# Optimization experiments

Hardware: AMD Instinct MI355X
Metric: run time of the kernel (lower is better)

Reference implementation:

```python
import jax, jax.numpy as jnp
import numpy as np

N_E = 8192
E_DIM = 512
BETA = 0.25


def setup_inputs() -> dict:
    key = jax.random.key(0)
    k1, k2, k3, k4, k5 = jax.random.split(key, 5)
    B, C, T = 8, E_DIM, 1024
    z = jax.random.normal(k1, (B, C, T), dtype=jnp.float32)
    # domain ids: 0 (speech), 1 (music), 2 (audio), 3 (no restriction / else-branch)
    audio_domain = jax.random.randint(k2, (B,), 0, 4, dtype=jnp.int64)
    # frozen codebook, init N(0, e_dim^-0.5) as in nn.init.normal_
    emb_weight = jax.random.normal(k3, (N_E, E_DIM), dtype=jnp.float32) * (E_DIM ** -0.5)
    # embedding_proj = nn.Linear(e_dim, e_dim): weight [out,in], bias [out]
    lim = 1.0 / np.sqrt(E_DIM)
    proj_w = jax.random.uniform(k4, (E_DIM, E_DIM), minval=-lim, maxval=lim, dtype=jnp.float32)
    proj_b = jax.random.uniform(k5, (E_DIM,), minval=-lim, maxval=lim, dtype=jnp.float32)
    return {"z": z, "audio_domain": audio_domain, "n_q": 1,
            "emb_weight": emb_weight, "proj_w": proj_w, "proj_b": proj_b}


def _domain_valid_mask(audio_domain):
    # valid[b, n] = True if code n is allowed for sample b
    cs = N_E // 4
    idx = jnp.arange(N_E)                      # [n_e]
    dom = audio_domain[:, None]                # [B, 1]
    m0 = idx < cs                              # domain 0: first quarter
    m1 = (idx >= cs) & (idx < 2 * cs)          # domain 1: second quarter
    m2 = idx >= 2 * cs                         # domain 2: last half
    valid = jnp.where(dom == 0, m0[None, :],
            jnp.where(dom == 1, m1[None, :],
            jnp.where(dom == 2, m2[None, :], True)))
    return valid                               # [B, n_e] bool


def reference(z, audio_domain, n_q, emb_weight, proj_w, proj_b):
    B, C, T = z.shape
    zt = jnp.transpose(z, (0, 2, 1))                       # [B, T, e_dim]
    zf = zt.reshape(-1, E_DIM)                              # [B*T, e_dim]
    # quant_codebook = Linear(embedding.weight)
    codebook = emb_weight @ proj_w.T + proj_b               # [n_e, e_dim]
    # squared euclidean distances via sum-sq + matmul
    d = (jnp.sum(zf * zf, axis=1, keepdims=True)
         + jnp.sum(codebook * codebook, axis=1)[None, :]
         - 2.0 * jnp.einsum('bd,nd->bn', zf, codebook))     # [B*T, n_e]
    d = d.reshape(B, T, N_E)
    valid = _domain_valid_mask(audio_domain)                # [B, n_e]
    d = jnp.where(valid[:, None, :], d, jnp.inf)
    min_idx = jnp.argmin(d, axis=2)                         # [B, T]
    z_q = codebook[min_idx]                                 # [B, T, e_dim]
    sg = jax.lax.stop_gradient
    # legacy=True commit loss
    commit_loss = (jnp.mean((sg(z_q) - zt) ** 2)
                   + BETA * jnp.mean((z_q - sg(zt)) ** 2))
    z_q = zt + sg(z_q - zt)                                 # straight-through
    z_q = jnp.transpose(z_q, (0, 2, 1))                     # [B, e_dim, T]
    min_idx = min_idx.reshape(1, B, T)                      # sane_index_shape
    return z_q, min_idx, commit_loss
```

## Files before the change

### kernel.cpp

```cpp
#include <hip/hip_runtime.h>
#include <math.h>

#define NE   8192
#define ED   512
#define BB   8
#define TT   1024
#define MM   (BB*TT)

#define FLT_BIG 3.402823466e38f
#define MARGIN  0.08f

typedef _Float16 half8 __attribute__((ext_vector_type(8)));
typedef _Float16 half4 __attribute__((ext_vector_type(4)));
typedef float    floatx4 __attribute__((ext_vector_type(4)));

typedef __attribute__((address_space(3))) unsigned int       lds_u32;
typedef const __attribute__((address_space(1))) unsigned int gbl_u32;

__device__ __forceinline__ void async_copy16(void* lds, const void* g) {
    __builtin_amdgcn_global_load_lds((gbl_u32*)(unsigned long long)g,
                                     (lds_u32*)(unsigned long long)lds,
                                     16, 0, 0);
}

__global__ __launch_bounds__(256) void k_prep(
    const float* __restrict__ z, const float* __restrict__ emb,
    const float* __restrict__ pw, _Float16* __restrict__ Zh,
    float* __restrict__ Zt, _Float16* __restrict__ Eb,
    _Float16* __restrict__ Wb, float* __restrict__ cnorm)
{
    const int bid = blockIdx.x;
    const int tid = threadIdx.x;
    if (bid < 1024) {
        __shared__ float T[64][68];
        const int ct = bid & 7, tt = (bid >> 3) & 15, b = bid >> 7;
        const int f4 = tid & 15;
        const int c0 = tid >> 4;
#pragma unroll
        for (int r = 0; r < 4; ++r) {
            const int c = c0 + r * 16;
            const float4 v = *(const float4*)(z + ((size_t)(b * ED + ct * 64 + c)) * TT + tt * 64 + f4 * 4);
            T[f4*4+0][c] = v.x; T[f4*4+1][c] = v.y;
            T[f4*4+2][c] = v.z; T[f4*4+3][c] = v.w;
        }
        __syncthreads();
        {
            const int tl = tid >> 2, q = tid & 3;
            const size_t m = (size_t)b * TT + tt * 64 + tl;
            _Float16* outh = Zh + m * 512 + ct * 64 + q * 16;
#pragma unroll
            for (int g = 0; g < 2; ++g) {
                half8 hv;
#pragma unroll
                for (int jj = 0; jj < 8; ++jj)
                    hv[jj] = (_Float16)(4.0f * T[tl][q*16 + g*8 + jj]);
                *(half8*)(outh + g * 8) = hv;
            }
        }
        {
            const int tl2 = tid >> 4;
            const int c4 = (tid & 15) * 4;
#pragma unroll
            for (int it = 0; it < 4; ++it) {
                const int t_local = tl2 + it * 16;
                const float4 v = *(const float4*)&T[t_local][c4];
                *(float4*)(Zt + ((size_t)b * TT + tt * 64 + t_local) * 512 + ct * 64 + c4) = v;
            }
        }
    } else if (bid < 5376) {
        const int g = (bid - 1024) * 256 + tid;
        const int row = g >> 7, c4 = (g & 127) * 4;
        const float* src;
        _Float16* dst;
        if (row < NE) { src = emb + (size_t)row * 512;        dst = Eb + (size_t)row * 1024; }
        else          { src = pw + (size_t)(row - NE) * 512;  dst = Wb + (size_t)(row - NE) * 1024; }
        const float4 v = *(const float4*)(src + c4);
        half4 h, l;
        const float s[4] = {v.x * 64.0f, v.y * 64.0f, v.z * 64.0f, v.w * 64.0f};
#pragma unroll
        for (int j = 0; j < 4; ++j) {
            const _Float16 hh = (_Float16)s[j];
            h[j] = hh;
            l[j] = (_Float16)(s[j] - (float)hh);
        }
        *(half4*)(dst + c4) = h;
        *(half4*)(dst + 512 + c4) = l;
    } else {
        const int zidx = bid - 5376;
        if (zidx < 8) {
            ((float4*)cnorm)[zidx * 256 + tid] = make_float4(0.f, 0.f, 0.f, 0.f);
        } else if (tid == 0) {
            cnorm[NE] = 0.0f;
            ((unsigned int*)cnorm)[NE + 1] = 0u;
        }
    }
}

#define S_AH 0
#define S_AL 8192
#define S_BH 16384
#define S_BL 20480
__global__ __launch_bounds__(256) void k_cb(
    const _Float16* __restrict__ Eb, const _Float16* __restrict__ Wb,
    const float* __restrict__ pb, float* __restrict__ cb,
    _Float16* __restrict__ Ch, float* __restrict__ cnorm)
{
    __shared__ __align__(16) _Float16 S[24576];

    const int tid = threadIdx.x;
    const int wave = tid >> 6, lane = tid & 63;
    const int n0 = blockIdx.x * 128, d0 = blockIdx.y * 64;
    const int wm = wave >> 1, wn = wave & 1;
    const int lm = lane & 15, lq = lane >> 4;

    floatx4 acc[4][2];
#pragma unroll
    for (int i = 0; i < 4; ++i)
#pragma unroll
        for (int j = 0; j < 2; ++j) acc[i][j] = (floatx4)0.0f;

    for (int lc = 0; lc < 8; ++lc) {
        const int kc = lc * 64;
        __syncthreads();
#pragma unroll
        for (int r = 0; r < 12; ++r) {
            const int s = wave * 12 + r;
            const int row8 = lane >> 3;
            const int srcx = lane & 7;
            if (s < 16) {
                const int row = s * 8 + row8;
                const int src = srcx ^ (row & 7);
                async_copy16(&S[S_AH + s * 512], Eb + (size_t)(n0 + row) * 1024 + kc + src * 8);
            } else if (s < 32) {
                const int s2 = s - 16;
                const int row = s2 * 8 + row8;
                const int src = srcx ^ (row & 7);
                async_copy16(&S[S_AL + s2 * 512], Eb + (size_t)(n0 + row) * 1024 + 512 + kc + src * 8);
            } else if (s < 40) {
                const int s2 = s - 32;
                const int row = s2 * 8 + row8;
                const int src = srcx ^ (row & 7);
                async_copy16(&S[S_BH + s2 * 512], Wb + (size_t)(d0 + row) * 1024 + kc + src * 8);
            } else {
                const int s2 = s - 40;
                const int row = s2 * 8 + row8;
                const int src = srcx ^ (row & 7);
                async_copy16(&S[S_BL + s2 * 512], Wb + (size_t)(d0 + row) * 1024 + 512 + kc + src * 8);
            }
        }
        __syncthreads();

#pragma unroll
        for (int ks = 0; ks < 2; ++ks) {
            half8 ah[4], al[4], bh[2], bl[2];
#pragma unroll
            for (int i = 0; i < 4; ++i) {
                const int row = wm * 64 + i * 16 + lm;
                const int slot = (ks * 4 + lq) ^ (row & 7);
                ah[i] = *(const half8*)&S[S_AH + row * 64 + slot * 8];
                al[i] = *(const half8*)&S[S_AL + row * 64 + slot * 8];
            }
#pragma unroll
            for (int j = 0; j < 2; ++j) {
                const int row = wn * 32 + j * 16 + lm;
                const int slot = (ks * 4 + lq) ^ (row & 7);
                bh[j] = *(const half8*)&S[S_BH + row * 64 + slot * 8];
                bl[j] = *(const half8*)&S[S_BL + row * 64 + slot * 8];
            }
#pragma unroll
            for (int i = 0; i < 4; ++i)
#pragma unroll
                for (int j = 0; j < 2; ++j) {
                    acc[i][j] = __builtin_amdgcn_mfma_f32_16x16x32_f16(ah[i], bh[j], acc[i][j], 0, 0, 0);
                    acc[i][j] = __builtin_amdgcn_mfma_f32_16x16x32_f16(ah[i], bl[j], acc[i][j], 0, 0, 0);
                    acc[i][j] = __builtin_amdgcn_mfma_f32_16x16x32_f16(al[i], bh[j], acc[i][j], 0, 0, 0);
                }
        }
    }

    float bias[2];
#pragma unroll
    for (int j = 0; j < 2; ++j) bias[j] = pb[d0 + wn * 32 + j * 16 + lm];

    float nsum[16];
#pragma unroll
    for (int p = 0; p < 16; ++p) nsum[p] = 0.0f;

#pragma unroll
    for (int i = 0; i < 4; ++i) {
#pragma unroll
        for (int j = 0; j < 2; ++j) {
            const int d = d0 + wn * 32 + j * 16 + lm;
#pragma unroll
            for (int r = 0; r < 4; ++r) {
                const float v = acc[i][j][r] * 0.000244140625f + bias[j];
                const int n = n0 + wm * 64 + i * 16 + lq * 4 + r;
                cb[(size_t)n * 512 + d] = v;
                Ch[(size_t)n * 512 + d] = (_Float16)(v * 64.0f);
                nsum[i * 4 + r] += v * v;
            }
        }
    }
#pragma unroll
    for (int stp = 1; stp < 16; stp <<= 1) {
#pragma unroll
        for (int p = 0; p < 16; ++p) nsum[p] += __shfl_xor(nsum[p], stp);
    }
    float myv = nsum[0];
#pragma unroll
    for (int p = 1; p < 16; ++p) if (lm == p) myv = nsum[p];
    const int n = n0 + wm * 64 + (lm >> 2) * 16 + lq * 4 + (lm & 3);
    atomicAdd(&cnorm[n], myv);
}

__global__ __launch_bounds__(256) void k_coarse(
    const _Float16* __restrict__ Zh, const _Float16* __restrict__ Ch,
    const float* __restrict__ cnorm, const int* __restrict__ dom_arr,
    _Float16* __restrict__ bmin)
{
    const int mt = blockIdx.x;
    const int nt = blockIdx.y;
    const int b = mt >> 3;
    const int dom = dom_arr[b];
    const int chunk = nt >> 4;
    const bool valid = (dom == 3) || (dom == 0 && chunk == 0) ||
                       (dom == 1 && chunk == 1) || (dom == 2 && chunk >= 2);

    const int tid = threadIdx.x;
    const int m0 = mt * 128, n0 = nt * 128;

    if (!valid) {
        const int r = tid >> 1, h = tid & 1;
        half8 v;
#pragma unroll
        for (int k = 0; k < 8; ++k) v[k] = (_Float16)65504.0f;
        *(half8*)(bmin + (size_t)(m0 + r) * 1024 + nt * 16 + h * 8) = v;
        return;
    }

    __shared__ __align__(16) _Float16 As[128 * 64];
    __shared__ __align__(16) _Float16 Bs[128 * 64];
    __shared__ __align__(16) _Float16 bs[128][20];
    __shared__ __align__(16) float cnLds[128];

    const int wave = tid >> 6, lane = tid & 63;
    const int wm = wave >> 1, wn = wave & 1;
    const int lm = lane & 15, lq = lane >> 4;

    floatx4 acc[4][4];
#pragma unroll
    for (int i = 0; i < 4; ++i)
#pragma unroll
        for (int j = 0; j < 4; ++j) acc[i][j] = (floatx4)0.0f;

    for (int lc = 0; lc < 8; ++lc) {
        const int kk0 = lc * 64;
        __syncthreads();
#pragma unroll
        for (int r = 0; r < 4; ++r) {
            const int s = wave * 4 + r;
            const int row = s * 8 + (lane >> 3);
            const int src = (lane & 7) ^ (row & 7);
            async_copy16(&As[s * 512], Ch + (size_t)(n0 + row) * 512 + kk0 + src * 8);
            async_copy16(&Bs[s * 512], Zh + (size_t)(m0 + row) * 512 + kk0 + src * 8);
        }
        if (lc == 0 && wave == 0 && lane < 32)
            async_copy16(&cnLds[0], cnorm + n0 + lane * 4);
        __syncthreads();

#pragma unroll
        for (int ks = 0; ks < 2; ++ks) {
            half8 af[4], bf[4];
#pragma unroll
            for (int i = 0; i < 4; ++i) {
                const int row = wm * 64 + i * 16 + lm;
                const int slot = (ks * 4 + lq) ^ (row & 7);
                af[i] = *(const half8*)&As[row * 64 + slot * 8];
            }
#pragma unroll
            for (int j = 0; j < 4; ++j) {
                const int row = wn * 64 + j * 16 + lm;
                const int slot = (ks * 4 + lq) ^ (row & 7);
                bf[j] = *(const half8*)&Bs[row * 64 + slot * 8];
            }
#pragma unroll
            for (int i = 0; i < 4; ++i)
#pragma unroll
                for (int j = 0; j < 4; ++j)
                    acc[i][j] = __builtin_amdgcn_mfma_f32_16x16x32_f16(af[i], bf[j], acc[i][j], 0, 0, 0);
        }
    }

    float cnv[4][4];
#pragma unroll
    for (int i = 0; i < 4; ++i)
#pragma unroll
        for (int r = 0; r < 4; ++r)
            cnv[i][r] = cnLds[wm * 64 + i * 16 + lq * 4 + r];

    float um[4][4];
#pragma unroll
    for (int i = 0; i < 4; ++i) {
#pragma unroll
        for (int j = 0; j < 4; ++j) {
            float m01 = fminf(cnv[i][0] - acc[i][j][0] * 0.0078125f,
                              cnv[i][1] - acc[i][j][1] * 0.0078125f);
            float m23 = fminf(cnv[i][2] - acc[i][j][2] * 0.0078125f,
                              cnv[i][3] - acc[i][j][3] * 0.0078125f);
            um[i][j] = fminf(m01, m23);
        }
    }
#pragma unroll
    for (int i = 0; i < 4; ++i)
#pragma unroll
        for (int j = 0; j < 4; ++j)
            um[i][j] = fminf(um[i][j], __shfl_xor(um[i][j], 16));

    if ((lq & 1) == 0) {
        const int p = lq >> 1;
#pragma unroll
        for (int i = 0; i < 4; ++i)
#pragma unroll
            for (int j = 0; j < 4; ++j)
                bs[wn * 64 + j * 16 + lm][wm * 8 + i * 2 + p] = (_Float16)um[i][j];
    }
    __syncthreads();
    {
        const int r = tid >> 1, h = tid & 1;
        half8 v;
#pragma unroll
        for (int k = 0; k < 8; ++k) v[k] = bs[r][h * 8 + k];
        *(half8*)(bmin + (size_t)(m0 + r) * 1024 + nt * 16 + h * 8) = v;
    }
}

__global__ __launch_bounds__(256) void k_refine(
    const float* __restrict__ Zt, const float* __restrict__ cb,
    const float* __restrict__ cnorm, const _Float16* __restrict__ bmin,
    int* __restrict__ minidx, float* __restrict__ out_idx)
{
    const int m = blockIdx.x * 4 + (threadIdx.x >> 6);
    const int lane = threadIdx.x & 63;

    const _Float16* brow = bmin + (size_t)m * 1024 + lane * 16;
    const half8 u0 = *(const half8*)brow;
    const half8 u1 = *(const half8*)(brow + 8);
    float um[16];
#pragma unroll
    for (int k = 0; k < 8; ++k) { um[k] = (float)u0[k]; um[8 + k] = (float)u1[k]; }

    float g = FLT_BIG;
#pragma unroll
    for (int k = 0; k < 16; ++k) g = fminf(g, um[k]);
#pragma unroll
    for (int s = 32; s > 0; s >>= 1) g = fminf(g, __shfl_xor(g, s));
    const float thr = g + MARGIN;

    float zr[8];
#pragma unroll
    for (int j = 0; j < 8; ++j)
        zr[j] = Zt[(size_t)m * 512 + lane + 64 * j];

    float bestv = FLT_BIG; int besti = 0;

    bool any = false;
#pragma unroll
    for (int k = 0; k < 16; ++k) any |= (um[k] <= thr);
    unsigned long long mask = __ballot(any);

    while (mask) {
        const int L = __ffsll(mask) - 1;
        mask &= mask - 1;
#pragma unroll
        for (int k = 0; k < 16; ++k) {
            const float uv = __shfl(um[k], L);
            if (!(uv <= thr)) continue;
            const int nbase = (L * 16 + k) * 8;
            for (int q = 0; q < 8; q += 2) {
                const float* r0 = cb + (size_t)(nbase + q) * 512 + lane;
                const float* r1 = r0 + 512;
                float d0 = 0.f, d1 = 0.f;
#pragma unroll
                for (int j = 0; j < 8; ++j) {
                    d0 += zr[j] * r0[64 * j];
                    d1 += zr[j] * r1[64 * j];
                }
#pragma unroll
                for (int s = 32; s > 0; s >>= 1) {
                    d0 += __shfl_xor(d0, s);
                    d1 += __shfl_xor(d1, s);
                }
                const float f0 = cnorm[nbase + q]     - 2.0f * d0;
                const float f1 = cnorm[nbase + q + 1] - 2.0f * d1;
                if (f0 < bestv) { bestv = f0; besti = nbase + q; }
                if (f1 < bestv) { bestv = f1; besti = nbase + q + 1; }
            }
        }
    }
    if (lane == 0) {
        minidx[m] = besti;
        out_idx[m] = (float)besti;
    }
}

#define ZQ_BLOCKS (4*16*8)
__global__ __launch_bounds__(256) void k_zq(
    const float* __restrict__ z, const float* __restrict__ cb,
    const int* __restrict__ minidx, float* __restrict__ outz,
    float* __restrict__ lossacc, unsigned int* __restrict__ donecnt,
    float* __restrict__ outloss)
{
    __shared__ float red[4];
    const int cc = blockIdx.x, tt = blockIdx.y, b = blockIdx.z;
    const int tl = threadIdx.x & 63;
    const int cg = threadIdx.x >> 6;
    const int t = tt * 64 + tl;
    const int idx = minidx[b * TT + t];
    const float* __restrict__ crow = cb + (size_t)idx * 512;

    float lsum = 0.f;
#pragma unroll 8
    for (int k = 0; k < 32; ++k) {
        const int c = cc * 128 + cg + k * 4;
        const float cv = crow[c];
        const size_t off = ((size_t)(b * ED + c)) * TT + t;
        const float zv = z[off];
        const float d = cv - zv;
        lsum += d * d;
        outz[off] = cv;
    }
#pragma unroll
    for (int off = 32; off > 0; off >>= 1) lsum += __shfl_down(lsum, off);
    if (tl == 0) red[threadIdx.x >> 6] = lsum;
    __syncthreads();
    if (threadIdx.x == 0) {
        atomicAdd(lossacc, red[0] + red[1] + red[2] + red[3]);
        __threadfence();
        const unsigned int old = atomicAdd(donecnt, 1u);
        if (old == ZQ_BLOCKS - 1) {
            const float total = atomicAdd(lossacc, 0.0f);
            *outloss = 1.25f * total / (float)(BB * ED * TT);
        }
    }
}

extern "C" void kernel_launch(void* const* d_in, const int* in_sizes, int n_in,
                              void* d_out, int out_size, void* d_ws, size_t ws_size,
                              hipStream_t stream)
{
    const float* z   = (const float*)d_in[0];
    const int*   dom = (const int*)d_in[1];
    const float* emb = (const float*)d_in[3];
    const float* pw  = (const float*)d_in[4];
    const float* pb  = (const float*)d_in[5];
    float* out = (float*)d_out;

    char* p = (char*)d_ws;
    _Float16* Zh = (_Float16*)p;            p += (size_t)MM * 512 * 2;
    float*    Zt = (float*)p;               p += (size_t)MM * 512 * 4;
    _Float16* Eb = (_Float16*)p;            p += (size_t)NE * 1024 * 2;
    _Float16* Wb = (_Float16*)p;            p += (size_t)ED * 1024 * 2;
    float*    cb = (float*)p;               p += (size_t)NE * 512 * 4;
    _Float16* Ch = (_Float16*)p;            p += (size_t)NE * 512 * 2;
    float* cnorm = (float*)p;               p += (size_t)NE * 4;
    float* lossacc = (float*)p;             p += 4;
    unsigned int* donecnt = (unsigned int*)p; p += 4;
    _Float16* bmin = (_Float16*)p;          p += (size_t)MM * 1024 * 2;
    int*   minidx = (int*)p;

    k_prep   <<<1024 + (NE + ED) / 2 + 9, 256, 0, stream>>>(z, emb, pw, Zh, Zt, Eb, Wb, cnorm);
    k_cb     <<<dim3(64, 8), 256, 0, stream>>>(Eb, Wb, pb, cb, Ch, cnorm);
    k_coarse <<<dim3(64, 64), 256, 0, stream>>>(Zh, Ch, cnorm, dom, bmin);
    k_refine <<<MM / 4, 256, 0, stream>>>(Zt, cb, cnorm, bmin, minidx, out + (size_t)NE * ED);
    k_zq     <<<dim3(4, 16, 8), 256, 0, stream>>>(z, cb, minidx, out, lossacc, donecnt,
                                                  out + (size_t)NE * ED + MM);
}
```

Measured before the change: 222.2 us.

## Refine coarse bucket granularity to 4 codes and skip invalid domain groups

The coarse kernel now writes a per-4-code bucket minimum (2048 per row) instead of per-8-code, and skips writing sentinel values for invalid domain tiles. The refine kernel reads the domain to scan only the valid quarter groups, and checks candidates in 4-code units. The aim is fewer exact fp32 distance evaluations and fewer wasted writes, at the cost of doubling the bmin buffer size and traffic for valid tiles. A tie-break on lower index is added to the argmin.

```diff
diff --git a/kernel.cpp b/kernel.cpp
--- a/kernel.cpp
+++ b/kernel.cpp
@@ -225,22 +225,13 @@
     const int chunk = nt >> 4;
     const bool valid = (dom == 3) || (dom == 0 && chunk == 0) ||
                        (dom == 1 && chunk == 1) || (dom == 2 && chunk >= 2);
+    if (!valid) return;
 
     const int tid = threadIdx.x;
     const int m0 = mt * 128, n0 = nt * 128;
 
-    if (!valid) {
-        const int r = tid >> 1, h = tid & 1;
-        half8 v;
-#pragma unroll
-        for (int k = 0; k < 8; ++k) v[k] = (_Float16)65504.0f;
-        *(half8*)(bmin + (size_t)(m0 + r) * 1024 + nt * 16 + h * 8) = v;
-        return;
-    }
-
     __shared__ __align__(16) _Float16 As[128 * 64];
     __shared__ __align__(16) _Float16 Bs[128 * 64];
-    __shared__ __align__(16) _Float16 bs[128][20];
     __shared__ __align__(16) float cnLds[128];
 
     const int wave = tid >> 6, lane = tid & 63;
@@ -310,90 +301,92 @@
             um[i][j] = fminf(m01, m23);
         }
     }
+
+    __syncthreads();
+    _Float16 (*bs)[40] = (_Float16(*)[40])As;
 #pragma unroll
     for (int i = 0; i < 4; ++i)
 #pragma unroll
         for (int j = 0; j < 4; ++j)
-            um[i][j] = fminf(um[i][j], __shfl_xor(um[i][j], 16));
-
-    if ((lq & 1) == 0) {
-        const int p = lq >> 1;
-#pragma unroll
-        for (int i = 0; i < 4; ++i)
-#pragma unroll
-            for (int j = 0; j < 4; ++j)
-                bs[wn * 64 + j * 16 + lm][wm * 8 + i * 2 + p] = (_Float16)um[i][j];
-    }
+            bs[wn * 64 + j * 16 + lm][wm * 16 + i * 4 + lq] = (_Float16)um[i][j];
     __syncthreads();
     {
         const int r = tid >> 1, h = tid & 1;
-        half8 v;
-#pragma unroll
-        for (int k = 0; k < 8; ++k) v[k] = bs[r][h * 8 + k];
-        *(half8*)(bmin + (size_t)(m0 + r) * 1024 + nt * 16 + h * 8) = v;
+        half8 v0, v1;
+#pragma unroll
+        for (int k = 0; k < 8; ++k) { v0[k] = bs[r][h * 16 + k]; v1[k] = bs[r][h * 16 + 8 + k]; }
+        _Float16* dst = bmin + (size_t)(m0 + r) * 2048 + nt * 32 + h * 16;
+        *(half8*)dst = v0;
+        *(half8*)(dst + 8) = v1;
     }
 }
 
 __global__ __launch_bounds__(256) void k_refine(
     const float* __restrict__ Zt, const float* __restrict__ cb,
     const float* __restrict__ cnorm, const _Float16* __restrict__ bmin,
-    int* __restrict__ minidx, float* __restrict__ out_idx)
+    const int* __restrict__ dom_arr, int* __restrict__ minidx,
+    float* __restrict__ out_idx)
 {
     const int m = blockIdx.x * 4 + (threadIdx.x >> 6);
     const int lane = threadIdx.x & 63;
-
-    const _Float16* brow = bmin + (size_t)m * 1024 + lane * 16;
-    const half8 u0 = *(const half8*)brow;
-    const half8 u1 = *(const half8*)(brow + 8);
-    float um[16];
-#pragma unroll
-    for (int k = 0; k < 8; ++k) { um[k] = (float)u0[k]; um[8 + k] = (float)u1[k]; }
-
-    float g = FLT_BIG;
-#pragma unroll
-    for (int k = 0; k < 16; ++k) g = fminf(g, um[k]);
-#pragma unroll
-    for (int s = 32; s > 0; s >>= 1) g = fminf(g, __shfl_xor(g, s));
-    const float thr = g + MARGIN;
+    const int b = m >> 10;
+    const int dom = dom_arr[b];
+    const int bg = (dom == 0) ? 0 : (dom == 1) ? 1 : (dom == 2) ? 2 : 0;
+    const int ng = (dom == 2) ? 2 : (dom == 3) ? 4 : 1;
+
+    const _Float16* brow = bmin + (size_t)m * 2048;
+    float um[4][8];
+    for (int g = 0; g < ng; ++g) {
+        const half8 u = *(const half8*)(brow + (bg + g) * 512 + lane * 8);
+#pragma unroll
+        for (int j = 0; j < 8; ++j) um[g][j] = (float)u[j];
+    }
+
+    float gmin = FLT_BIG;
+    for (int g = 0; g < ng; ++g)
+#pragma unroll
+        for (int j = 0; j < 8; ++j) gmin = fminf(gmin, um[g][j]);
+#pragma unroll
+    for (int s = 32; s > 0; s >>= 1) gmin = fminf(gmin, __shfl_xor(gmin, s));
+    const float thr = gmin + MARGIN;
 
     float zr[8];
 #pragma unroll
     for (int j = 0; j < 8; ++j)
         zr[j] = Zt[(size_t)m * 512 + lane + 64 * j];
 
-    float bestv = FLT_BIG; int besti = 0;
-
-    bool any = false;
-#pragma unroll
-    for (int k = 0; k < 16; ++k) any |= (um[k] <= thr);
-    unsigned long long mask = __ballot(any);
-
-    while (mask) {
-        const int L = __ffsll(mask) - 1;
-        mask &= mask - 1;
-#pragma unroll
-        for (int k = 0; k < 16; ++k) {
-            const float uv = __shfl(um[k], L);
-            if (!(uv <= thr)) continue;
-            const int nbase = (L * 16 + k) * 8;
-            for (int q = 0; q < 8; q += 2) {
-                const float* r0 = cb + (size_t)(nbase + q) * 512 + lane;
-                const float* r1 = r0 + 512;
-                float d0 = 0.f, d1 = 0.f;
-#pragma unroll
-                for (int j = 0; j < 8; ++j) {
-                    d0 += zr[j] * r0[64 * j];
-                    d1 += zr[j] * r1[64 * j];
+    float bestv = FLT_BIG; int besti = 0x7FFFFFFF;
+
+    for (int g = 0; g < ng; ++g) {
+#pragma unroll
+        for (int j = 0; j < 8; ++j) {
+            unsigned long long mask = __ballot(um[g][j] <= thr);
+            while (mask) {
+                const int L = __ffsll(mask) - 1;
+                mask &= mask - 1;
+                const int unit = (bg + g) * 512 + L * 8 + j;
+                const int nbase = unit * 4;
+#pragma unroll
+                for (int q = 0; q < 4; q += 2) {
+                    const float* r0 = cb + (size_t)(nbase + q) * 512 + lane;
+                    const float* r1 = r0 + 512;
+                    float d0 = 0.f, d1 = 0.f;
+#pragma unroll
+                    for (int jj = 0; jj < 8; ++jj) {
+                        d0 += zr[jj] * r0[64 * jj];
+                        d1 += zr[jj] * r1[64 * jj];
+                    }
+#pragma unroll
+                    for (int s = 32; s > 0; s >>= 1) {
+                        d0 += __shfl_xor(d0, s);
+                        d1 += __shfl_xor(d1, s);
+                    }
+                    const float f0 = cnorm[nbase + q]     - 2.0f * d0;
+                    const float f1 = cnorm[nbase + q + 1] - 2.0f * d1;
+                    const int n0i = nbase + q, n1i = nbase + q + 1;
+                    if (f0 < bestv || (f0 == bestv && n0i < besti)) { bestv = f0; besti = n0i; }
+                    if (f1 < bestv || (f1 == bestv && n1i < besti)) { bestv = f1; besti = n1i; }
                 }
-#pragma unroll
-                for (int s = 32; s > 0; s >>= 1) {
-                    d0 += __shfl_xor(d0, s);
-                    d1 += __shfl_xor(d1, s);
-                }
-                const float f0 = cnorm[nbase + q]     - 2.0f * d0;
-                const float f1 = cnorm[nbase + q + 1] - 2.0f * d1;
-                if (f0 < bestv) { bestv = f0; besti = nbase + q; }
-                if (f1 < bestv) { bestv = f1; besti = nbase + q + 1; }
             }
         }
     }
@@ -465,13 +458,13 @@
     float* cnorm = (float*)p;               p += (size_t)NE * 4;
     float* lossacc = (float*)p;             p += 4;
     unsigned int* donecnt = (unsigned int*)p; p += 4;
-    _Float16* bmin = (_Float16*)p;          p += (size_t)MM * 1024 * 2;
+    _Float16* bmin = (_Float16*)p;          p += (size_t)MM * 2048 * 2;
     int*   minidx = (int*)p;
 
     k_prep   <<<1024 + (NE + ED) / 2 + 9, 256, 0, stream>>>(z, emb, pw, Zh, Zt, Eb, Wb, cnorm);
     k_cb     <<<dim3(64, 8), 256, 0, stream>>>(Eb, Wb, pb, cb, Ch, cnorm);
     k_coarse <<<dim3(64, 64), 256, 0, stream>>>(Zh, Ch, cnorm, dom, bmin);
-    k_refine <<<MM / 4, 256, 0, stream>>>(Zt, cb, cnorm, bmin, minidx, out + (size_t)NE * ED);
+    k_refine <<<MM / 4, 256, 0, stream>>>(Zt, cb, cnorm, bmin, dom, minidx, out + (size_t)NE * ED);
     k_zq     <<<dim3(4, 16, 8), 256, 0, stream>>>(z, cb, minidx, out, lossacc, donecnt,
                                                   out + (size_t)NE * ED + MM);
 }
```

Result: faster. 213.3 us (-4.0%).
